# Kernel optimization log

Hardware: AMD Instinct MI355X
Metric: run time of the kernel (lower is better)

## Reference

```python
import jax, jax.numpy as jnp
import numpy as np

KH, KW = 3, 3  # kernel_size


def _median_patches(x):
    """tf.image.extract_patches(SAME, stride 1) + top_k median over k*k*C values.
    Returns [B, H, W, 1] with the (D//2+1)-th largest value per window (D = KH*KW*C),
    exactly matching tf.nn.top_k(..., k=D//2+1).values[..., -1]."""
    B, H, W, C = x.shape
    ph, pw = KH - 1, KW - 1  # SAME padding, stride 1
    xp = jnp.pad(x, ((0, 0), (ph // 2, ph - ph // 2), (pw // 2, pw - pw // 2), (0, 0)))
    # [B, H, W, KH*KW, C] via shifted slices (zero-padded borders, like TF SAME)
    patches = jnp.stack(
        [xp[:, i:i + H, j:j + W, :] for i in range(KH) for j in range(KW)], axis=3
    )
    D = KH * KW * C
    patches = patches.reshape(B, H, W, D)
    # k-th largest with k = D//2 + 1  ->  ascending-sorted index D - (D//2 + 1)
    med_idx = D - (D // 2) - 1
    med = jnp.sort(patches, axis=-1)[..., med_idx]
    return med[..., None]


def setup_inputs() -> dict:
    key = jax.random.key(0)
    kx, kw = jax.random.split(key)
    x = jax.random.normal(kx, (32, 224, 224, 3), dtype=jnp.float32)
    W = jax.random.normal(kw, (KH, KW, 1, 64), dtype=jnp.float32) * 0.1  # HWIO, in_ch=1
    return {"x": x, "W": W}


def reference(x, W):
    med = _median_patches(x)                              # [B, H, W, 1]
    med = med - jnp.mean(med, axis=(0, 1, 2), keepdims=True)  # global mean-center
    out = jax.lax.conv_general_dilated(
        med, W, window_strides=(1, 1), padding="SAME",
        dimension_numbers=("NHWC", "HWIO", "NHWC"),
    )                                                      # [B, H, W, num_filters]
    return out
```

## Files before the change

kernel.cpp:

```cpp
#include <hip/hip_runtime.h>

#define BB 32
#define HH 224
#define WW 224
#define CC 3
#define FF 64
#define NPIX (BB * HH * WW)
#define NOUT ((long long)NPIX * FF)

#define PH 226
#define PW 228
#define PB (PH * PW)
#define NPAD (BB * PB)
#define NBLK_MED (NPAD / 256)

typedef float f32x4 __attribute__((ext_vector_type(4)));
typedef float f32x4u __attribute__((ext_vector_type(4), aligned(4)));

__global__ __launch_bounds__(256) void median_pad_kernel(const float* __restrict__ x,
                                                         float* __restrict__ cmed,
                                                         float* __restrict__ partial) {
    const int idx = blockIdx.x * 256 + threadIdx.x;
    const int b  = idx / PB;
    const int r  = idx % PB;
    const int hp = r / PW;
    const int wp = r % PW;

    float m = 0.0f;
    if (hp >= 1 && hp <= HH && wp >= 1 && wp <= WW) {
        const int h = hp - 1;
        const int w = wp - 1;
        float v[27];
        #pragma unroll
        for (int i = 0; i < 3; ++i) {
            const int hh = h + i - 1;
            #pragma unroll
            for (int j = 0; j < 3; ++j) {
                const int ww = w + j - 1;
                const bool ok = (hh >= 0) && (hh < HH) && (ww >= 0) && (ww < WW);
                const float* p = x + (((long long)b * HH + hh) * WW + ww) * CC;
                #pragma unroll
                for (int c = 0; c < CC; ++c) {
                    v[(i * 3 + j) * 3 + c] = ok ? p[c] : 0.0f;
                }
            }
        }
        #pragma unroll
        for (int k = 0; k <= 13; ++k) {
            #pragma unroll
            for (int j = k + 1; j < 27; ++j) {
                const float lo = fminf(v[k], v[j]);
                const float hi = fmaxf(v[k], v[j]);
                v[k] = lo;
                v[j] = hi;
            }
        }
        m = v[13];
    }
    cmed[idx] = m;

    __shared__ float sdata[256];
    sdata[threadIdx.x] = m;
    __syncthreads();
    #pragma unroll
    for (int s = 128; s > 0; s >>= 1) {
        if (threadIdx.x < s) sdata[threadIdx.x] += sdata[threadIdx.x + s];
        __syncthreads();
    }
    if (threadIdx.x == 0) partial[blockIdx.x] = sdata[0];
}

__global__ __launch_bounds__(256) void mean_wsum_kernel(const float* __restrict__ partial,
                                                        const float* __restrict__ Wt,
                                                        float* __restrict__ mean_out,
                                                        float* __restrict__ Asum) {
    if (threadIdx.x < FF) {
        float s = 0.0f;
        #pragma unroll
        for (int t = 0; t < 9; ++t) s += Wt[t * FF + threadIdx.x];
        Asum[threadIdx.x] = s;
    }
    float s = 0.0f;
    for (int i = threadIdx.x; i < NBLK_MED; i += 256) s += partial[i];
    __shared__ float sdata[256];
    sdata[threadIdx.x] = s;
    __syncthreads();
    #pragma unroll
    for (int st = 128; st > 0; st >>= 1) {
        if (threadIdx.x < st) sdata[threadIdx.x] += sdata[threadIdx.x + st];
        __syncthreads();
    }
    if (threadIdx.x == 0) mean_out[0] = sdata[0] / (float)NPIX;
}

__global__ __launch_bounds__(256) void conv_kernel(const float* __restrict__ cmed,
                                                   const float* __restrict__ Wt,
                                                   const float* __restrict__ Asum,
                                                   const float* __restrict__ mean_p,
                                                   float* __restrict__ out) {
    const int bid = blockIdx.x;
    const int h  = bid % HH;
    const int b  = bid / HH;

    const int fg = threadIdx.x & 15;
    const int pg = threadIdx.x >> 4;
    const int f4 = fg * 4;

    float w[9][4];
    #pragma unroll
    for (int t = 0; t < 9; ++t) {
        const f32x4u wv = *(const f32x4u*)(Wt + t * FF + f4);
        w[t][0] = wv.x; w[t][1] = wv.y; w[t][2] = wv.z; w[t][3] = wv.w;
    }
    const f32x4u Av = *(const f32x4u*)(Asum + f4);
    const float mean = mean_p[0];

    const float* base = cmed + ((long long)b * PH + h) * PW;
    f32x4u cv[7][3];
    #pragma unroll
    for (int it = 0; it < 7; ++it) {
        #pragma unroll
        for (int r = 0; r < 3; ++r) {
            cv[it][r] = *(const f32x4u*)(base + r * PW + it * 32 + pg * 2);
        }
    }

    float Sb[4] = {Av.x, Av.y, Av.z, Av.w};
    if (h == 0) {
        #pragma unroll
        for (int k = 0; k < 4; ++k) Sb[k] -= (w[0][k] + w[1][k] + w[2][k]);
    }
    if (h == HH - 1) {
        #pragma unroll
        for (int k = 0; k < 4; ++k) Sb[k] -= (w[6][k] + w[7][k] + w[8][k]);
    }

    float* orow = out + (((long long)b * HH + h) * WW) * FF + f4;

    #pragma unroll
    for (int it = 0; it < 7; ++it) {
        const int p = it * 32 + pg * 2;

        float acc0[4] = {0.f, 0.f, 0.f, 0.f};
        float acc1[4] = {0.f, 0.f, 0.f, 0.f};
        #pragma unroll
        for (int r = 0; r < 3; ++r) {
            const f32x4u cvv = cv[it][r];
            #pragma unroll
            for (int k = 0; k < 4; ++k) {
                acc0[k] = fmaf(cvv.x, w[r * 3 + 0][k], acc0[k]);
                acc0[k] = fmaf(cvv.y, w[r * 3 + 1][k], acc0[k]);
                acc0[k] = fmaf(cvv.z, w[r * 3 + 2][k], acc0[k]);
                acc1[k] = fmaf(cvv.y, w[r * 3 + 0][k], acc1[k]);
                acc1[k] = fmaf(cvv.z, w[r * 3 + 1][k], acc1[k]);
                acc1[k] = fmaf(cvv.w, w[r * 3 + 2][k], acc1[k]);
            }
        }

        float S0[4], S1[4];
        #pragma unroll
        for (int k = 0; k < 4; ++k) { S0[k] = Sb[k]; S1[k] = Sb[k]; }
        if (it == 0 && pg == 0) {
            #pragma unroll
            for (int k = 0; k < 4; ++k) {
                S0[k] -= (w[0][k] + w[3][k] + w[6][k]);
                if (h == 0)      S0[k] += w[0][k];
                if (h == HH - 1) S0[k] += w[6][k];
            }
        }
        if (it == 6 && pg == 15) {
            #pragma unroll
            for (int k = 0; k < 4; ++k) {
                S1[k] -= (w[2][k] + w[5][k] + w[8][k]);
                if (h == 0)      S1[k] += w[2][k];
                if (h == HH - 1) S1[k] += w[8][k];
            }
        }

        f32x4 o0, o1;
        o0.x = fmaf(-mean, S0[0], acc0[0]); o0.y = fmaf(-mean, S0[1], acc0[1]);
        o0.z = fmaf(-mean, S0[2], acc0[2]); o0.w = fmaf(-mean, S0[3], acc0[3]);
        o1.x = fmaf(-mean, S1[0], acc1[0]); o1.y = fmaf(-mean, S1[1], acc1[1]);
        o1.z = fmaf(-mean, S1[2], acc1[2]); o1.w = fmaf(-mean, S1[3], acc1[3]);

        float* op = orow + (long long)p * FF;
        __builtin_nontemporal_store(o0, (f32x4*)op);
        __builtin_nontemporal_store(o1, (f32x4*)(op + FF));
    }
}

extern "C" void kernel_launch(void* const* d_in, const int* in_sizes, int n_in,
                              void* d_out, int out_size, void* d_ws, size_t ws_size,
                              hipStream_t stream) {
    const float* x  = (const float*)d_in[0];
    const float* Wt = (const float*)d_in[1];
    float* out = (float*)d_out;

    float* cmed    = (float*)d_ws;
    float* Asum    = cmed + NPAD;
    float* partial = Asum + FF;
    float* mean_p  = partial + NBLK_MED;

    median_pad_kernel<<<NBLK_MED, 256, 0, stream>>>(x, cmed, partial);
    mean_wsum_kernel<<<1, 256, 0, stream>>>(partial, Wt, mean_p, Asum);

    const int nblk_conv = BB * HH;
    conv_kernel<<<nblk_conv, 256, 0, stream>>>(cmed, Wt, Asum, mean_p, out);
}
```

Measured before the change: 125.7 us.

## Share column-sorted triples across sliding windows for median selection network

The median kernel now has each thread handle 7 adjacent pixels in a row. It pre-sorts each 3x3-channel column of 9 values once, then derives each window median by merging three sorted columns with a pruned network. This replaces the full 27-element partial selection sort per pixel and cuts the min/max operations and redundant global loads. Zeroing of the padding border moves into the mean-reduction kernel as extra blocks. The cost is higher register pressure from the col[9][9] array and more complex correctness reasoning for the selection network.

```diff
diff --git a/kernel.cpp b/kernel.cpp
--- a/kernel.cpp
+++ b/kernel.cpp
@@ -6,91 +6,167 @@
 #define CC 3
 #define FF 64
 #define NPIX (BB * HH * WW)
-#define NOUT ((long long)NPIX * FF)
 
 #define PH 226
 #define PW 228
 #define PB (PH * PW)
 #define NPAD (BB * PB)
-#define NBLK_MED (NPAD / 256)
 
 typedef float f32x4 __attribute__((ext_vector_type(4)));
 typedef float f32x4u __attribute__((ext_vector_type(4), aligned(4)));
 
-__global__ __launch_bounds__(256) void median_pad_kernel(const float* __restrict__ x,
+#define CEX(A,B) { const float _lo = fminf(A,B); B = fmaxf(A,B); A = _lo; }
+
+__global__ __launch_bounds__(128) void median_pad_kernel(const float* __restrict__ x,
                                                          float* __restrict__ cmed,
                                                          float* __restrict__ partial) {
-    const int idx = blockIdx.x * 256 + threadIdx.x;
-    const int b  = idx / PB;
-    const int r  = idx % PB;
-    const int hp = r / PW;
-    const int wp = r % PW;
-
-    float m = 0.0f;
-    if (hp >= 1 && hp <= HH && wp >= 1 && wp <= WW) {
-        const int h = hp - 1;
-        const int w = wp - 1;
-        float v[27];
-        #pragma unroll
-        for (int i = 0; i < 3; ++i) {
-            const int hh = h + i - 1;
-            #pragma unroll
-            for (int j = 0; j < 3; ++j) {
-                const int ww = w + j - 1;
-                const bool ok = (hh >= 0) && (hh < HH) && (ww >= 0) && (ww < WW);
-                const float* p = x + (((long long)b * HH + hh) * WW + ww) * CC;
-                #pragma unroll
-                for (int c = 0; c < CC; ++c) {
-                    v[(i * 3 + j) * 3 + c] = ok ? p[c] : 0.0f;
-                }
-            }
-        }
-        #pragma unroll
-        for (int k = 0; k <= 13; ++k) {
-            #pragma unroll
-            for (int j = k + 1; j < 27; ++j) {
-                const float lo = fminf(v[k], v[j]);
-                const float hi = fmaxf(v[k], v[j]);
-                v[k] = lo;
-                v[j] = hi;
-            }
-        }
-        m = v[13];
-    }
-    cmed[idx] = m;
-
-    __shared__ float sdata[256];
-    sdata[threadIdx.x] = m;
+    const int bid = blockIdx.x;
+    const int b  = bid / 56;
+    const int hg = bid % 56;
+    const int h  = hg * 4 + (threadIdx.x >> 5);
+    const int s  = threadIdx.x & 31;
+    const int w0 = s * 7;
+
+    const bool okT = (h > 0);
+    const bool okB = (h < HH - 1);
+    const float* r0p = x + (((long long)b * HH + (okT ? h - 1 : 0)) * WW) * CC;
+    const float* r1p = x + (((long long)b * HH + h) * WW) * CC;
+    const float* r2p = x + (((long long)b * HH + (okB ? h + 1 : 0)) * WW) * CC;
+
+    float col[9][9];
+
+#define COLSTEP(CS) { \
+    const int wcol = w0 - 1 + (CS); \
+    const bool vw = (wcol >= 0) && (wcol < WW); \
+    const int off3 = (vw ? wcol : 0) * CC; \
+    const bool v0 = vw && okT, v1 = vw, v2 = vw && okB; \
+    float a0 = v0 ? r0p[off3+0] : 0.f, a1 = v0 ? r0p[off3+1] : 0.f, a2 = v0 ? r0p[off3+2] : 0.f; \
+    float b0 = v1 ? r1p[off3+0] : 0.f, b1 = v1 ? r1p[off3+1] : 0.f, b2 = v1 ? r1p[off3+2] : 0.f; \
+    float c0 = v2 ? r2p[off3+0] : 0.f, c1 = v2 ? r2p[off3+1] : 0.f, c2 = v2 ? r2p[off3+2] : 0.f; \
+    CEX(a0,a1); CEX(a1,a2); CEX(a0,a1);         \
+    CEX(b0,b1); CEX(b1,b2); CEX(b0,b1);         \
+    CEX(c0,c1); CEX(c1,c2); CEX(c0,c1);         \
+     \
+    float s0 = a0, L = b0; CEX(s0, L); \
+    float s5 = b2, Hh = a2; CEX(Hh, s5); \
+    float q0 = L, q1 = a1, q2 = b1, q3 = Hh; \
+    CEX(q0,q1); CEX(q2,q3); CEX(q0,q2); CEX(q1,q3); CEX(q1,q2); \
+     \
+    float z0 = s0, p = c0; CEX(z0, p); \
+    float z8 = c2, qq = s5; CEX(qq, z8); \
+    float t0 = p, t1 = c1, t2 = qq; CEX(t0,t1); CEX(t1,t2); CEX(t0,t1); \
+    float m1 = q0, u = t0; CEX(m1, u); \
+    float m7 = t2, vvv = q3; CEX(vvv, m7); \
+    float e0 = u, e1 = q1, e2 = q2; CEX(e0,e1); CEX(e1,e2); \
+    float f0 = t1, f1 = e0, f2 = e1, f3 = e2; CEX(f0,f1); CEX(f1,f2); CEX(f2,f3); \
+    float g0 = vvv, g1 = f0, g2 = f1, g3 = f2, g4 = f3; \
+    CEX(g0,g1); CEX(g1,g2); CEX(g2,g3); CEX(g3,g4); \
+    col[CS][0]=z0; col[CS][1]=m1; col[CS][2]=g0; col[CS][3]=g1; col[CS][4]=g2; \
+    col[CS][5]=g3; col[CS][6]=g4; col[CS][7]=m7; col[CS][8]=z8; }
+
+    COLSTEP(0) COLSTEP(1) COLSTEP(2) COLSTEP(3) COLSTEP(4)
+    COLSTEP(5) COLSTEP(6) COLSTEP(7) COLSTEP(8)
+
+    float med[7];
+    float lsum = 0.f;
+
+#define MEDSTEP(O) { \
+     \
+    float x0 = col[O][0], y0 = col[O+2][0]; CEX(x0, y0);    \
+    float x8 = col[O][8], y8 = col[O+2][8]; CEX(x8, y8);    \
+    float g0 = y0, g1 = col[O][1], g2 = col[O][2], g3 = col[O][3], \
+          g4 = col[O][4], g5 = col[O][5], g6 = col[O][6], g7 = col[O][7]; \
+    CEX(g0,g1); CEX(g1,g2); CEX(g2,g3); CEX(g3,g4); CEX(g4,g5); CEX(g5,g6); CEX(g6,g7); \
+    float h0 = col[O+2][1], h1 = col[O+2][2], h2 = col[O+2][3], h3 = col[O+2][4], \
+          h4 = col[O+2][5], h5 = col[O+2][6], h6 = col[O+2][7], h7 = x8; \
+    CEX(h6,h7); CEX(h5,h6); CEX(h4,h5); CEX(h3,h4); CEX(h2,h3); CEX(h1,h2); CEX(h0,h1); \
+     \
+    float Ea = g0, Eb = g4, Ec = h0, Ed = h4; \
+    float Ea2 = g2, Eb2 = g6, Ec2 = h2, Ed2 = h6; \
+    CEX(Ea,Ec); CEX(Eb,Ed); CEX(Eb,Ec); \
+    CEX(Ea2,Ec2); CEX(Eb2,Ed2); CEX(Eb2,Ec2); \
+    CEX(Ea2,Eb); CEX(Eb2,Ec); CEX(Ec2,Ed); \
+     \
+    float Fa = g1, Fb = g5, Fc = h1, Fd = h5; \
+    float Fa2 = g3, Fb2 = g7, Fc2 = h3, Fd2 = h7; \
+    CEX(Fa,Fc); CEX(Fb,Fd); CEX(Fb,Fc); \
+    CEX(Fa2,Fc2); CEX(Fb2,Fd2); CEX(Fb2,Fc2); \
+    CEX(Fa2,Fb); CEX(Fb2,Fc); CEX(Fc2,Fd); \
+     \
+    float M3 = Fa2, M4 = Eb;  CEX(M3, M4);    \
+    float M5 = Fb,  M6 = Eb2; CEX(M5, M6);    \
+    float M7 = Fb2, M8 = Ec;  CEX(M7, M8);    \
+    float M9 = Fc,  M10 = Ec2; CEX(M9, M10);  \
+    float M11 = Fc2, M12 = Ed; CEX(M11, M12); \
+    float r = fminf(fmaxf(M3, col[O+1][8]), fmaxf(M4, col[O+1][7])); \
+    r = fminf(r, fmaxf(M5, col[O+1][6])); \
+    r = fminf(r, fmaxf(M6, col[O+1][5])); \
+    r = fminf(r, fmaxf(M7, col[O+1][4])); \
+    r = fminf(r, fmaxf(M8, col[O+1][3])); \
+    r = fminf(r, fmaxf(M9, col[O+1][2])); \
+    r = fminf(r, fmaxf(M10, col[O+1][1])); \
+    r = fminf(r, fmaxf(M11, col[O+1][0])); \
+    r = fminf(r, M12); \
+    med[O] = r; lsum += r; }
+
+    MEDSTEP(0) MEDSTEP(1) MEDSTEP(2) MEDSTEP(3) MEDSTEP(4) MEDSTEP(5) MEDSTEP(6)
+
+    float* crow = cmed + ((long long)b * PH + (h + 1)) * PW + (w0 + 1);
+    crow[0] = med[0]; crow[1] = med[1]; crow[2] = med[2]; crow[3] = med[3];
+    crow[4] = med[4]; crow[5] = med[5]; crow[6] = med[6];
+
+    __shared__ float sdata[128];
+    sdata[threadIdx.x] = lsum;
     __syncthreads();
     #pragma unroll
-    for (int s = 128; s > 0; s >>= 1) {
-        if (threadIdx.x < s) sdata[threadIdx.x] += sdata[threadIdx.x + s];
-        __syncthreads();
-    }
-    if (threadIdx.x == 0) partial[blockIdx.x] = sdata[0];
-}
-
-__global__ __launch_bounds__(256) void mean_wsum_kernel(const float* __restrict__ partial,
-                                                        const float* __restrict__ Wt,
-                                                        float* __restrict__ mean_out,
-                                                        float* __restrict__ Asum) {
-    if (threadIdx.x < FF) {
-        float s = 0.0f;
-        #pragma unroll
-        for (int t = 0; t < 9; ++t) s += Wt[t * FF + threadIdx.x];
-        Asum[threadIdx.x] = s;
-    }
-    float s = 0.0f;
-    for (int i = threadIdx.x; i < NBLK_MED; i += 256) s += partial[i];
-    __shared__ float sdata[256];
-    sdata[threadIdx.x] = s;
-    __syncthreads();
-    #pragma unroll
-    for (int st = 128; st > 0; st >>= 1) {
+    for (int st = 64; st > 0; st >>= 1) {
         if (threadIdx.x < st) sdata[threadIdx.x] += sdata[threadIdx.x + st];
         __syncthreads();
     }
-    if (threadIdx.x == 0) mean_out[0] = sdata[0] / (float)NPIX;
+    if (threadIdx.x == 0) partial[blockIdx.x] = sdata[0];
+}
+
+__global__ __launch_bounds__(256) void mean_wsum_border_kernel(const float* __restrict__ partial,
+                                                               const float* __restrict__ Wt,
+                                                               float* __restrict__ mean_out,
+                                                               float* __restrict__ Asum,
+                                                               float* __restrict__ cmed) {
+    if (blockIdx.x == 0) {
+        if (threadIdx.x < FF) {
+            float s = 0.0f;
+            #pragma unroll
+            for (int t = 0; t < 9; ++t) s += Wt[t * FF + threadIdx.x];
+            Asum[threadIdx.x] = s;
+        }
+        float s = 0.0f;
+        for (int i = threadIdx.x; i < 1792; i += 256) s += partial[i];
+        __shared__ float sdata[256];
+        sdata[threadIdx.x] = s;
+        __syncthreads();
+        #pragma unroll
+        for (int st = 128; st > 0; st >>= 1) {
+            if (threadIdx.x < st) sdata[threadIdx.x] += sdata[threadIdx.x + st];
+            __syncthreads();
+        }
+        if (threadIdx.x == 0) mean_out[0] = sdata[0] / (float)NPIX;
+    } else {
+        const int u = (blockIdx.x - 1) * 256 + threadIdx.x;
+        int b, hp, wp;
+        if (u < 14592) {
+            b = u / 456;
+            const int v = u % 456;
+            hp = (v < 228) ? 0 : (PH - 1);
+            wp = (v < 228) ? v : (v - 228);
+        } else {
+            const int u2 = u - 14592;
+            b = u2 / 896;
+            const int v2 = u2 % 896;
+            hp = 1 + (v2 % 224);
+            const int j = v2 / 224;
+            wp = (j == 0) ? 0 : (224 + j);
+        }
+        cmed[((long long)b * PH + hp) * PW + wp] = 0.0f;
+    }
 }
 
 __global__ __launch_bounds__(256) void conv_kernel(const float* __restrict__ cmed,
@@ -199,11 +275,9 @@
     float* cmed    = (float*)d_ws;
     float* Asum    = cmed + NPAD;
     float* partial = Asum + FF;
-    float* mean_p  = partial + NBLK_MED;
-
-    median_pad_kernel<<<NBLK_MED, 256, 0, stream>>>(x, cmed, partial);
-    mean_wsum_kernel<<<1, 256, 0, stream>>>(partial, Wt, mean_p, Asum);
-
-    const int nblk_conv = BB * HH;
-    conv_kernel<<<nblk_conv, 256, 0, stream>>>(cmed, Wt, Asum, mean_p, out);
-}
+    float* mean_p  = partial + 1792;
+
+    median_pad_kernel<<<1792, 128, 0, stream>>>(x, cmed, partial);
+    mean_wsum_border_kernel<<<170, 256, 0, stream>>>(partial, Wt, mean_p, Asum, cmed);
+    conv_kernel<<<BB * HH, 256, 0, stream>>>(cmed, Wt, Asum, mean_p, out);
+}
```

Result: faster. 115.1 us (-8.5%).
